# Optimization experiments

Measured on AMD Instinct MI355X. Metric: run time of the kernel, lower is better.

Reference implementation:

```python
import jax, jax.numpy as jnp
import numpy as np
import math

HIDDEN = 1024
HEADS = 16
HEAD_DIM = HIDDEN // HEADS
B, S = 2, 2048


def setup_inputs() -> dict:
    key = jax.random.key(0)
    ks = jax.random.split(key, 10)
    std = 1.0 / math.sqrt(HIDDEN)
    mk = lambda k: (jax.random.normal(k, (HIDDEN, HIDDEN), jnp.float32) * std)
    return {
        "hidden_states": jax.random.normal(ks[0], (B, S, HIDDEN), jnp.float32),
        "attention_mask": jnp.zeros((B, 1, 1, S), jnp.float32),
        "wq": mk(ks[1]), "bq": jnp.zeros((HIDDEN,), jnp.float32),
        "wk": mk(ks[2]), "bk": jnp.zeros((HIDDEN,), jnp.float32),
        "wv": mk(ks[3]), "bv": jnp.zeros((HIDDEN,), jnp.float32),
        "wo": mk(ks[4]), "bo": jnp.zeros((HIDDEN,), jnp.float32),
    }


def reference(hidden_states, attention_mask, wq, bq, wk, bk, wv, bv, wo, bo):
    b, s, _ = hidden_states.shape
    scale = math.sqrt(HEAD_DIM)
    # projections (torch Linear: x @ W.T + b); weights stored as [out, in]
    q = hidden_states @ wq.T + bq
    k = hidden_states @ wk.T + bk
    v = hidden_states @ wv.T + bv
    # [B, H, S, D]
    q = q.reshape(b, s, HEADS, HEAD_DIM).transpose(0, 2, 1, 3)
    k = k.reshape(b, s, HEADS, HEAD_DIM).transpose(0, 2, 1, 3)
    v = v.reshape(b, s, HEADS, HEAD_DIM).transpose(0, 2, 1, 3)
    scores = jnp.einsum("bhqd,bhkd->bhqk", q, k) / scale
    scores = scores + attention_mask  # broadcast [B,1,1,S]
    weights = jax.nn.softmax(scores, axis=-1)  # dropout = identity (eval)
    out = jnp.einsum("bhqk,bhkd->bhqd", weights, v)
    out = out.transpose(0, 2, 1, 3).reshape(b, s, HIDDEN)
    out = out @ wo.T + bo
    return out
```

## Files before the change

### kernel.cpp

```cpp
#include <hip/hip_runtime.h>
#include <hip/hip_bf16.h>

typedef __bf16 bf16_t;
typedef __bf16 bf16x8 __attribute__((ext_vector_type(8)));
typedef float f32x4 __attribute__((ext_vector_type(4)));

#define SEQ    2048
#define NH     16
#define HD     64
#define HIDDEN 1024
#define PSTR   72

__device__ __forceinline__ bf16_t to_bf16(float f) { return (bf16_t)f; }

__device__ __forceinline__ void async16(const bf16_t* g, bf16_t* l) {
    __builtin_amdgcn_global_load_lds((const __attribute__((address_space(1))) void*)g,
                                     (__attribute__((address_space(3))) void*)l, 16, 0, 0);
}

__global__ __launch_bounds__(256) void cvt_kernel(
    const float* __restrict__ s0, bf16_t* __restrict__ d0, int c0,
    const float* __restrict__ s1, bf16_t* __restrict__ d1, int c1,
    const float* __restrict__ s2, bf16_t* __restrict__ d2, int c2,
    const float* __restrict__ s3, bf16_t* __restrict__ d3, int c3)
{
    int blk = blockIdx.x;
    const float* s; bf16_t* d;
    if (blk < c0)              { s = s0; d = d0; }
    else if ((blk -= c0) < c1) { s = s1; d = d1; }
    else if ((blk -= c1) < c2) { s = s2; d = d2; }
    else                       { blk -= c2; s = s3; d = d3; }
    const size_t base = (size_t)blk * 2048 + threadIdx.x * 8;
    const float4 a = *(const float4*)&s[base];
    const float4 b = *(const float4*)&s[base + 4];
    bf16x8 o;
    o[0] = (bf16_t)a.x; o[1] = (bf16_t)a.y; o[2] = (bf16_t)a.z; o[3] = (bf16_t)a.w;
    o[4] = (bf16_t)b.x; o[5] = (bf16_t)b.y; o[6] = (bf16_t)b.z; o[7] = (bf16_t)b.w;
    *(bf16x8*)&d[base] = o;
}

__device__ __forceinline__ void gemm_tile(const bf16_t* __restrict__ A,
                                          const bf16_t* __restrict__ W,
                                          int m0, int n0, f32x4 acc[4][4])
{
    __shared__ __align__(16) bf16_t As[128 * 32];
    __shared__ __align__(16) bf16_t Bs[128 * 32];
    const int t = threadIdx.x, lane = t & 63, w = t >> 6;
    const int w0 = w & 1, w1 = w >> 1, l15 = lane & 15, q4 = lane >> 4;

#pragma unroll
    for (int i = 0; i < 4; i++)
#pragma unroll
        for (int j = 0; j < 4; j++) acc[i][j] = f32x4{0.f, 0.f, 0.f, 0.f};

    for (int kt = 0; kt < HIDDEN; kt += 32) {
#pragma unroll
        for (int j = 0; j < 2; j++) {
            const int s = j * 256 + t;
            const int row = s >> 2, p = s & 3, c = p ^ (row & 3);
            const int lbase = (j * 256 + w * 64) * 8;
            async16(&A[(size_t)(m0 + row) * HIDDEN + kt + c * 8], &As[lbase]);
            async16(&W[(size_t)(n0 + row) * HIDDEN + kt + c * 8], &Bs[lbase]);
        }
        __syncthreads();
        bf16x8 af[4];
#pragma unroll
        for (int ti = 0; ti < 4; ti++) {
            const int r = w0 * 64 + ti * 16 + l15;
            af[ti] = *(const bf16x8*)&As[r * 32 + (q4 ^ (r & 3)) * 8];
        }
#pragma unroll
        for (int tj = 0; tj < 4; tj++) {
            const int rb = w1 * 64 + tj * 16 + l15;
            const bf16x8 bfr = *(const bf16x8*)&Bs[rb * 32 + (q4 ^ (rb & 3)) * 8];
#pragma unroll
            for (int ti = 0; ti < 4; ti++)
                acc[ti][tj] = __builtin_amdgcn_mfma_f32_16x16x32_bf16(af[ti], bfr, acc[ti][tj], 0, 0, 0);
        }
        __syncthreads();
    }
}

__global__ __launch_bounds__(256, 3) void qkv_kernel(
    const bf16_t* __restrict__ X,
    const bf16_t* __restrict__ wq, const bf16_t* __restrict__ wk, const bf16_t* __restrict__ wv,
    const float* __restrict__ bq, const float* __restrict__ bk, const float* __restrict__ bv,
    bf16_t* __restrict__ qws, bf16_t* __restrict__ kws, bf16_t* __restrict__ vws)
{
    const int z = blockIdx.z;
    const bf16_t* Wsel = (z == 0) ? wq : (z == 1) ? wk : wv;
    const float*  bsel = (z == 0) ? bq : (z == 1) ? bk : bv;
    bf16_t* dst        = (z == 0) ? qws : (z == 1) ? kws : vws;
    const int m0 = blockIdx.y * 128, n0 = blockIdx.x * 128;

    f32x4 acc[4][4];
    gemm_tile(X, Wsel, m0, n0, acc);

    const int t = threadIdx.x, lane = t & 63, wv_ = t >> 6;
    const int w0 = wv_ & 1, w1 = wv_ >> 1, l15 = lane & 15, q4 = lane >> 4;
#pragma unroll
    for (int tj = 0; tj < 4; tj++) {
        const int n = n0 + w1 * 64 + tj * 16 + l15;
        const float bb = bsel[n];
        const int hh = n >> 6, d = n & 63;
#pragma unroll
        for (int ti = 0; ti < 4; ti++)
#pragma unroll
            for (int r = 0; r < 4; r++) {
                const int m = m0 + w0 * 64 + ti * 16 + q4 * 4 + r;
                const int b = m >> 11, s = m & (SEQ - 1);
                const float val = acc[ti][tj][r] + bb;
                if (z < 2)
                    dst[(((size_t)b * NH + hh) * SEQ + s) * HD + d] = to_bf16(val);
                else
                    dst[(((size_t)b * NH + hh) * HD + d) * SEQ + s] = to_bf16(val);
            }
    }
}

__global__ __launch_bounds__(256, 4) void attn_kernel(
    const bf16_t* __restrict__ Qw, const bf16_t* __restrict__ Kw,
    const bf16_t* __restrict__ Vtw, const float* __restrict__ Mask,
    bf16_t* __restrict__ Ow)
{
    __shared__ __align__(16) bf16_t Ks[64 * 64];
    __shared__ __align__(16) bf16_t Vs[64 * 64];
    __shared__ __align__(16) bf16_t Ps[4 * 16 * PSTR];

    const int t = threadIdx.x, lane = t & 63, w = t >> 6;
    const int l15 = lane & 15, q4 = lane >> 4;
    const int bh = blockIdx.y, b = bh >> 4, h = bh & 15;
    const int q0 = blockIdx.x * 64;
    const bf16_t* Qh = Qw  + (size_t)bh * SEQ * HD;
    const bf16_t* Kh = Kw  + (size_t)bh * SEQ * HD;
    const bf16_t* Vh = Vtw + (size_t)bh * HD * SEQ;
    const float* Mrow = Mask + (size_t)b * SEQ;

    bf16x8 qf[2];
#pragma unroll
    for (int ks = 0; ks < 2; ks++)
        qf[ks] = *(const bf16x8*)&Qh[(size_t)(q0 + w * 16 + l15) * HD + ks * 32 + q4 * 8];

    f32x4 oacc[4];
#pragma unroll
    for (int nb = 0; nb < 4; nb++) oacc[nb] = f32x4{0.f, 0.f, 0.f, 0.f};
    float psum[4] = {0.f, 0.f, 0.f, 0.f};

    for (int kt = 0; kt < SEQ; kt += 64) {
#pragma unroll
        for (int j = 0; j < 2; j++) {
            const int s = j * 256 + t;
            const int row = s >> 3, p = s & 7, c = p ^ (row & 7);
            const int lbase = (j * 256 + w * 64) * 8;
            async16(&Kh[(size_t)(kt + row) * HD + c * 8], &Ks[lbase]);
            async16(&Vh[(size_t)row * SEQ + kt + c * 8], &Vs[lbase]);
        }
        __syncthreads();

        f32x4 sa[4];
#pragma unroll
        for (int cb = 0; cb < 4; cb++) sa[cb] = f32x4{0.f, 0.f, 0.f, 0.f};
#pragma unroll
        for (int cb = 0; cb < 4; cb++)
#pragma unroll
            for (int ks = 0; ks < 2; ks++) {
                const int r = cb * 16 + l15;
                const bf16x8 kf = *(const bf16x8*)&Ks[r * 64 + (((ks * 4 + q4) ^ (r & 7))) * 8];
                sa[cb] = __builtin_amdgcn_mfma_f32_16x16x32_bf16(qf[ks], kf, sa[cb], 0, 0, 0);
            }

#pragma unroll
        for (int cb = 0; cb < 4; cb++) {
            const float mk = Mrow[kt + cb * 16 + l15];
#pragma unroll
            for (int r = 0; r < 4; r++) {
                const float p = __expf(sa[cb][r] * 0.125f + mk);
                psum[r] += p;
                Ps[(w * 16 + q4 * 4 + r) * PSTR + cb * 16 + l15] = to_bf16(p);
            }
        }

#pragma unroll
        for (int ks = 0; ks < 2; ks++) {
            const bf16x8 pf = *(const bf16x8*)&Ps[(w * 16 + l15) * PSTR + ks * 32 + q4 * 8];
#pragma unroll
            for (int nb = 0; nb < 4; nb++) {
                const int r = nb * 16 + l15;
                const bf16x8 vf = *(const bf16x8*)&Vs[r * 64 + (((ks * 4 + q4) ^ (r & 7))) * 8];
                oacc[nb] = __builtin_amdgcn_mfma_f32_16x16x32_bf16(pf, vf, oacc[nb], 0, 0, 0);
            }
        }
        __syncthreads();
    }

#pragma unroll
    for (int r = 0; r < 4; r++) {
#pragma unroll
        for (int off = 1; off < 16; off <<= 1) psum[r] += __shfl_xor(psum[r], off);
    }
#pragma unroll
    for (int r = 0; r < 4; r++) {
        const float inv = 1.f / psum[r];
        const int s = q0 + w * 16 + q4 * 4 + r;
#pragma unroll
        for (int nb = 0; nb < 4; nb++) {
            const int d = nb * 16 + l15;
            Ow[((size_t)b * SEQ + s) * HIDDEN + h * HD + d] = to_bf16(oacc[nb][r] * inv);
        }
    }
}

__global__ __launch_bounds__(256, 3) void oproj_kernel(
    const bf16_t* __restrict__ A, const bf16_t* __restrict__ Wo,
    const float* __restrict__ bo, float* __restrict__ Out)
{
    const int m0 = blockIdx.y * 128, n0 = blockIdx.x * 128;
    f32x4 acc[4][4];
    gemm_tile(A, Wo, m0, n0, acc);
    const int t = threadIdx.x, lane = t & 63, wv_ = t >> 6;
    const int w0 = wv_ & 1, w1 = wv_ >> 1, l15 = lane & 15, q4 = lane >> 4;
#pragma unroll
    for (int tj = 0; tj < 4; tj++) {
        const int n = n0 + w1 * 64 + tj * 16 + l15;
        const float bb = bo[n];
#pragma unroll
        for (int ti = 0; ti < 4; ti++)
#pragma unroll
            for (int r = 0; r < 4; r++) {
                const int m = m0 + w0 * 64 + ti * 16 + q4 * 4 + r;
                Out[(size_t)m * HIDDEN + n] = acc[ti][tj][r] + bb;
            }
    }
}

extern "C" void kernel_launch(void* const* d_in, const int* in_sizes, int n_in,
                              void* d_out, int out_size, void* d_ws, size_t ws_size,
                              hipStream_t stream) {
    const float* X   = (const float*)d_in[0];
    const float* msk = (const float*)d_in[1];
    const float* wq  = (const float*)d_in[2];
    const float* bq  = (const float*)d_in[3];
    const float* wk  = (const float*)d_in[4];
    const float* bk  = (const float*)d_in[5];
    const float* wv  = (const float*)d_in[6];
    const float* bv  = (const float*)d_in[7];
    const float* wo  = (const float*)d_in[8];
    const float* bo  = (const float*)d_in[9];
    float* out = (float*)d_out;

    const size_t NELT = (size_t)2 * SEQ * HIDDEN;
    const size_t WELT = (size_t)HIDDEN * HIDDEN;
    bf16_t* xbf = (bf16_t*)d_ws;
    bf16_t* qws = xbf + NELT;
    bf16_t* kws = qws + NELT;
    bf16_t* vws = kws + NELT;
    bf16_t* aws = xbf;
    bf16_t* wqb = (bf16_t*)d_out;
    bf16_t* wkb = wqb + WELT;
    bf16_t* wvb = wkb + WELT;
    bf16_t* wob = qws;

    cvt_kernel<<<dim3(2048 + 3 * 512), dim3(256), 0, stream>>>(
        X, xbf, 2048, wq, wqb, 512, wk, wkb, 512, wv, wvb, 512);
    qkv_kernel<<<dim3(8, 32, 3), dim3(256), 0, stream>>>(
        xbf, wqb, wkb, wvb, bq, bk, bv, qws, kws, vws);
    attn_kernel<<<dim3(32, 32), dim3(256), 0, stream>>>(qws, kws, vws, msk, aws);
    cvt_kernel<<<dim3(512), dim3(256), 0, stream>>>(
        wo, wob, 512, wo, wob, 0, wo, wob, 0, wo, wob, 0);
    oproj_kernel<<<dim3(8, 32), dim3(256), 0, stream>>>(aws, wob, bo, out);
}
```

Measured before the change: 222.1 us.

## Retile QKV/oproj GEMMs and attention, store Q/K row-major, use exp2

Result: slower. 229.5 us (+3.3%).

```diff
diff --git a/kernel.cpp b/kernel.cpp
--- a/kernel.cpp
+++ b/kernel.cpp
@@ -10,6 +10,7 @@
 #define HD     64
 #define HIDDEN 1024
 #define PSTR   72
+#define LOG2E  1.44269504f
 
 __device__ __forceinline__ bf16_t to_bf16(float f) { return (bf16_t)f; }
 
@@ -39,65 +40,59 @@
     *(bf16x8*)&d[base] = o;
 }
 
-__device__ __forceinline__ void gemm_tile(const bf16_t* __restrict__ A,
-                                          const bf16_t* __restrict__ W,
-                                          int m0, int n0, f32x4 acc[4][4])
-{
-    __shared__ __align__(16) bf16_t As[128 * 32];
-    __shared__ __align__(16) bf16_t Bs[128 * 32];
-    const int t = threadIdx.x, lane = t & 63, w = t >> 6;
-    const int w0 = w & 1, w1 = w >> 1, l15 = lane & 15, q4 = lane >> 4;
-
-#pragma unroll
-    for (int i = 0; i < 4; i++)
-#pragma unroll
-        for (int j = 0; j < 4; j++) acc[i][j] = f32x4{0.f, 0.f, 0.f, 0.f};
-
-    for (int kt = 0; kt < HIDDEN; kt += 32) {
-#pragma unroll
-        for (int j = 0; j < 2; j++) {
-            const int s = j * 256 + t;
-            const int row = s >> 2, p = s & 3, c = p ^ (row & 3);
-            const int lbase = (j * 256 + w * 64) * 8;
-            async16(&A[(size_t)(m0 + row) * HIDDEN + kt + c * 8], &As[lbase]);
-            async16(&W[(size_t)(n0 + row) * HIDDEN + kt + c * 8], &Bs[lbase]);
-        }
-        __syncthreads();
-        bf16x8 af[4];
-#pragma unroll
-        for (int ti = 0; ti < 4; ti++) {
-            const int r = w0 * 64 + ti * 16 + l15;
-            af[ti] = *(const bf16x8*)&As[r * 32 + (q4 ^ (r & 3)) * 8];
-        }
-#pragma unroll
-        for (int tj = 0; tj < 4; tj++) {
-            const int rb = w1 * 64 + tj * 16 + l15;
-            const bf16x8 bfr = *(const bf16x8*)&Bs[rb * 32 + (q4 ^ (rb & 3)) * 8];
-#pragma unroll
-            for (int ti = 0; ti < 4; ti++)
-                acc[ti][tj] = __builtin_amdgcn_mfma_f32_16x16x32_bf16(af[ti], bfr, acc[ti][tj], 0, 0, 0);
-        }
-        __syncthreads();
-    }
-}
-
 __global__ __launch_bounds__(256, 3) void qkv_kernel(
     const bf16_t* __restrict__ X,
     const bf16_t* __restrict__ wq, const bf16_t* __restrict__ wk, const bf16_t* __restrict__ wv,
     const float* __restrict__ bq, const float* __restrict__ bk, const float* __restrict__ bv,
     bf16_t* __restrict__ qws, bf16_t* __restrict__ kws, bf16_t* __restrict__ vws)
 {
+    __shared__ __align__(16) bf16_t As[128 * 64];
+    __shared__ __align__(16) bf16_t Bs[128 * 64];
     const int z = blockIdx.z;
     const bf16_t* Wsel = (z == 0) ? wq : (z == 1) ? wk : wv;
     const float*  bsel = (z == 0) ? bq : (z == 1) ? bk : bv;
     bf16_t* dst        = (z == 0) ? qws : (z == 1) ? kws : vws;
     const int m0 = blockIdx.y * 128, n0 = blockIdx.x * 128;
 
+    const int t = threadIdx.x, lane = t & 63, w = t >> 6;
+    const int w0 = w & 1, w1 = w >> 1, l15 = lane & 15, q4 = lane >> 4;
+
     f32x4 acc[4][4];
-    gemm_tile(X, Wsel, m0, n0, acc);
-
-    const int t = threadIdx.x, lane = t & 63, wv_ = t >> 6;
-    const int w0 = wv_ & 1, w1 = wv_ >> 1, l15 = lane & 15, q4 = lane >> 4;
+#pragma unroll
+    for (int i = 0; i < 4; i++)
+#pragma unroll
+        for (int j = 0; j < 4; j++) acc[i][j] = f32x4{0.f, 0.f, 0.f, 0.f};
+
+    for (int kt = 0; kt < HIDDEN; kt += 64) {
+#pragma unroll
+        for (int j = 0; j < 4; j++) {
+            const int s = j * 256 + t;
+            const int row = s >> 3, c = (s & 7) ^ (row & 7);
+            const int lbase = (j * 256 + w * 64) * 8;
+            async16(&X[(size_t)(m0 + row) * HIDDEN + kt + c * 8], &As[lbase]);
+            async16(&Wsel[(size_t)(n0 + row) * HIDDEN + kt + c * 8], &Bs[lbase]);
+        }
+        __syncthreads();
+#pragma unroll
+        for (int ks = 0; ks < 2; ks++) {
+            bf16x8 af[4];
+#pragma unroll
+            for (int ti = 0; ti < 4; ti++) {
+                const int ra = w0 * 64 + ti * 16 + l15;
+                af[ti] = *(const bf16x8*)&As[ra * 64 + (((ks * 4 + q4) ^ (ra & 7))) * 8];
+            }
+#pragma unroll
+            for (int tj = 0; tj < 4; tj++) {
+                const int rb = w1 * 64 + tj * 16 + l15;
+                const bf16x8 bfr = *(const bf16x8*)&Bs[rb * 64 + (((ks * 4 + q4) ^ (rb & 7))) * 8];
+#pragma unroll
+                for (int ti = 0; ti < 4; ti++)
+                    acc[ti][tj] = __builtin_amdgcn_mfma_f32_16x16x32_bf16(af[ti], bfr, acc[ti][tj], 0, 0, 0);
+            }
+        }
+        __syncthreads();
+    }
+
 #pragma unroll
     for (int tj = 0; tj < 4; tj++) {
         const int n = n0 + w1 * 64 + tj * 16 + l15;
@@ -108,126 +103,187 @@
 #pragma unroll
             for (int r = 0; r < 4; r++) {
                 const int m = m0 + w0 * 64 + ti * 16 + q4 * 4 + r;
-                const int b = m >> 11, s = m & (SEQ - 1);
                 const float val = acc[ti][tj][r] + bb;
-                if (z < 2)
-                    dst[(((size_t)b * NH + hh) * SEQ + s) * HD + d] = to_bf16(val);
-                else
+                if (z < 2) {
+                    dst[(size_t)m * HIDDEN + n] = to_bf16(val);
+                } else {
+                    const int b = m >> 11, s = m & (SEQ - 1);
                     dst[(((size_t)b * NH + hh) * HD + d) * SEQ + s] = to_bf16(val);
-            }
-    }
-}
-
-__global__ __launch_bounds__(256, 4) void attn_kernel(
+                }
+            }
+    }
+}
+
+__global__ __launch_bounds__(256, 2) void attn_kernel(
     const bf16_t* __restrict__ Qw, const bf16_t* __restrict__ Kw,
     const bf16_t* __restrict__ Vtw, const float* __restrict__ Mask,
     bf16_t* __restrict__ Ow)
 {
     __shared__ __align__(16) bf16_t Ks[64 * 64];
     __shared__ __align__(16) bf16_t Vs[64 * 64];
-    __shared__ __align__(16) bf16_t Ps[4 * 16 * PSTR];
+    __shared__ __align__(16) bf16_t Ps[4 * 32 * PSTR];
 
     const int t = threadIdx.x, lane = t & 63, w = t >> 6;
     const int l15 = lane & 15, q4 = lane >> 4;
-    const int bh = blockIdx.y, b = bh >> 4, h = bh & 15;
-    const int q0 = blockIdx.x * 64;
-    const bf16_t* Qh = Qw  + (size_t)bh * SEQ * HD;
-    const bf16_t* Kh = Kw  + (size_t)bh * SEQ * HD;
+    const int lid = blockIdx.x + 16 * blockIdx.y;
+    const int c8 = lid & 7, j = lid >> 3;
+    const int bh = (c8 << 2) | (j >> 4);
+    const int q0 = (j & 15) << 7;
+    const int b = bh >> 4, h = bh & 15;
+
+    const bf16_t* Qh = Qw + (size_t)b * SEQ * HIDDEN + h * HD;
+    const bf16_t* Kh = Kw + (size_t)b * SEQ * HIDDEN + h * HD;
     const bf16_t* Vh = Vtw + (size_t)bh * HD * SEQ;
     const float* Mrow = Mask + (size_t)b * SEQ;
 
-    bf16x8 qf[2];
-#pragma unroll
-    for (int ks = 0; ks < 2; ks++)
-        qf[ks] = *(const bf16x8*)&Qh[(size_t)(q0 + w * 16 + l15) * HD + ks * 32 + q4 * 8];
-
-    f32x4 oacc[4];
-#pragma unroll
-    for (int nb = 0; nb < 4; nb++) oacc[nb] = f32x4{0.f, 0.f, 0.f, 0.f};
-    float psum[4] = {0.f, 0.f, 0.f, 0.f};
+    bf16x8 qf[2][2];
+#pragma unroll
+    for (int rb = 0; rb < 2; rb++)
+#pragma unroll
+        for (int ks = 0; ks < 2; ks++)
+            qf[rb][ks] = *(const bf16x8*)&Qh[(size_t)(q0 + w * 32 + rb * 16 + l15) * HIDDEN + ks * 32 + q4 * 8];
+
+    f32x4 oacc[2][4];
+#pragma unroll
+    for (int rb = 0; rb < 2; rb++)
+#pragma unroll
+        for (int nb = 0; nb < 4; nb++) oacc[rb][nb] = f32x4{0.f, 0.f, 0.f, 0.f};
+    float psum[2][4] = {{0.f, 0.f, 0.f, 0.f}, {0.f, 0.f, 0.f, 0.f}};
 
     for (int kt = 0; kt < SEQ; kt += 64) {
 #pragma unroll
-        for (int j = 0; j < 2; j++) {
-            const int s = j * 256 + t;
-            const int row = s >> 3, p = s & 7, c = p ^ (row & 7);
-            const int lbase = (j * 256 + w * 64) * 8;
-            async16(&Kh[(size_t)(kt + row) * HD + c * 8], &Ks[lbase]);
+        for (int jj = 0; jj < 2; jj++) {
+            const int s = jj * 256 + t;
+            const int row = s >> 3, c = (s & 7) ^ (row & 7);
+            const int lbase = (jj * 256 + w * 64) * 8;
+            async16(&Kh[(size_t)(kt + row) * HIDDEN + c * 8], &Ks[lbase]);
             async16(&Vh[(size_t)row * SEQ + kt + c * 8], &Vs[lbase]);
         }
         __syncthreads();
 
-        f32x4 sa[4];
-#pragma unroll
-        for (int cb = 0; cb < 4; cb++) sa[cb] = f32x4{0.f, 0.f, 0.f, 0.f};
+        f32x4 sa[2][4];
+#pragma unroll
+        for (int rb = 0; rb < 2; rb++)
+#pragma unroll
+            for (int cb = 0; cb < 4; cb++) sa[rb][cb] = f32x4{0.f, 0.f, 0.f, 0.f};
 #pragma unroll
         for (int cb = 0; cb < 4; cb++)
 #pragma unroll
             for (int ks = 0; ks < 2; ks++) {
                 const int r = cb * 16 + l15;
                 const bf16x8 kf = *(const bf16x8*)&Ks[r * 64 + (((ks * 4 + q4) ^ (r & 7))) * 8];
-                sa[cb] = __builtin_amdgcn_mfma_f32_16x16x32_bf16(qf[ks], kf, sa[cb], 0, 0, 0);
+                sa[0][cb] = __builtin_amdgcn_mfma_f32_16x16x32_bf16(qf[0][ks], kf, sa[0][cb], 0, 0, 0);
+                sa[1][cb] = __builtin_amdgcn_mfma_f32_16x16x32_bf16(qf[1][ks], kf, sa[1][cb], 0, 0, 0);
             }
 
 #pragma unroll
         for (int cb = 0; cb < 4; cb++) {
-            const float mk = Mrow[kt + cb * 16 + l15];
-#pragma unroll
-            for (int r = 0; r < 4; r++) {
-                const float p = __expf(sa[cb][r] * 0.125f + mk);
-                psum[r] += p;
-                Ps[(w * 16 + q4 * 4 + r) * PSTR + cb * 16 + l15] = to_bf16(p);
-            }
+            const float mk2 = Mrow[kt + cb * 16 + l15] * LOG2E;
+#pragma unroll
+            for (int rb = 0; rb < 2; rb++)
+#pragma unroll
+                for (int r = 0; r < 4; r++) {
+                    const float p = exp2f(fmaf(sa[rb][cb][r], 0.125f * LOG2E, mk2));
+                    psum[rb][r] += p;
+                    Ps[(w * 32 + rb * 16 + q4 * 4 + r) * PSTR + cb * 16 + l15] = to_bf16(p);
+                }
         }
 
 #pragma unroll
         for (int ks = 0; ks < 2; ks++) {
-            const bf16x8 pf = *(const bf16x8*)&Ps[(w * 16 + l15) * PSTR + ks * 32 + q4 * 8];
+            const bf16x8 pf0 = *(const bf16x8*)&Ps[(w * 32 +      l15) * PSTR + ks * 32 + q4 * 8];
+            const bf16x8 pf1 = *(const bf16x8*)&Ps[(w * 32 + 16 + l15) * PSTR + ks * 32 + q4 * 8];
 #pragma unroll
             for (int nb = 0; nb < 4; nb++) {
-                const int r = nb * 16 + l15;
-                const bf16x8 vf = *(const bf16x8*)&Vs[r * 64 + (((ks * 4 + q4) ^ (r & 7))) * 8];
-                oacc[nb] = __builtin_amdgcn_mfma_f32_16x16x32_bf16(pf, vf, oacc[nb], 0, 0, 0);
-            }
-        }
-        __syncthreads();
-    }
-
-#pragma unroll
-    for (int r = 0; r < 4; r++) {
-#pragma unroll
-        for (int off = 1; off < 16; off <<= 1) psum[r] += __shfl_xor(psum[r], off);
-    }
-#pragma unroll
-    for (int r = 0; r < 4; r++) {
-        const float inv = 1.f / psum[r];
-        const int s = q0 + w * 16 + q4 * 4 + r;
-#pragma unroll
-        for (int nb = 0; nb < 4; nb++) {
-            const int d = nb * 16 + l15;
-            Ow[((size_t)b * SEQ + s) * HIDDEN + h * HD + d] = to_bf16(oacc[nb][r] * inv);
-        }
-    }
-}
-
-__global__ __launch_bounds__(256, 3) void oproj_kernel(
+                const int rv = nb * 16 + l15;
+                const bf16x8 vf = *(const bf16x8*)&Vs[rv * 64 + (((ks * 4 + q4) ^ (rv & 7))) * 8];
+                oacc[0][nb] = __builtin_amdgcn_mfma_f32_16x16x32_bf16(pf0, vf, oacc[0][nb], 0, 0, 0);
+                oacc[1][nb] = __builtin_amdgcn_mfma_f32_16x16x32_bf16(pf1, vf, oacc[1][nb], 0, 0, 0);
+            }
+        }
+        __syncthreads();
+    }
+
+#pragma unroll
+    for (int rb = 0; rb < 2; rb++)
+#pragma unroll
+        for (int r = 0; r < 4; r++) {
+#pragma unroll
+            for (int off = 1; off < 16; off <<= 1) psum[rb][r] += __shfl_xor(psum[rb][r], off);
+        }
+#pragma unroll
+    for (int rb = 0; rb < 2; rb++)
+#pragma unroll
+        for (int r = 0; r < 4; r++) {
+            const float inv = 1.f / psum[rb][r];
+            const int s = q0 + w * 32 + rb * 16 + q4 * 4 + r;
+#pragma unroll
+            for (int nb = 0; nb < 4; nb++) {
+                const int d = nb * 16 + l15;
+                Ow[((size_t)b * SEQ + s) * HIDDEN + h * HD + d] = to_bf16(oacc[rb][nb][r] * inv);
+            }
+        }
+}
+
+__global__ __launch_bounds__(256, 2) void oproj_kernel(
     const bf16_t* __restrict__ A, const bf16_t* __restrict__ Wo,
     const float* __restrict__ bo, float* __restrict__ Out)
 {
-    const int m0 = blockIdx.y * 128, n0 = blockIdx.x * 128;
-    f32x4 acc[4][4];
-    gemm_tile(A, Wo, m0, n0, acc);
-    const int t = threadIdx.x, lane = t & 63, wv_ = t >> 6;
-    const int w0 = wv_ & 1, w1 = wv_ >> 1, l15 = lane & 15, q4 = lane >> 4;
-#pragma unroll
-    for (int tj = 0; tj < 4; tj++) {
-        const int n = n0 + w1 * 64 + tj * 16 + l15;
+    __shared__ __align__(16) bf16_t As[64 * 64];
+    __shared__ __align__(16) bf16_t Bs[128 * 64];
+    const int m0 = blockIdx.y * 64, n0 = blockIdx.x * 128;
+    const int t = threadIdx.x, lane = t & 63, w = t >> 6;
+    const int l15 = lane & 15, q4 = lane >> 4;
+
+    f32x4 acc[4][2];
+#pragma unroll
+    for (int i = 0; i < 4; i++)
+#pragma unroll
+        for (int j = 0; j < 2; j++) acc[i][j] = f32x4{0.f, 0.f, 0.f, 0.f};
+
+    for (int kt = 0; kt < HIDDEN; kt += 64) {
+#pragma unroll
+        for (int j = 0; j < 2; j++) {
+            const int s = j * 256 + t;
+            const int row = s >> 3, c = (s & 7) ^ (row & 7);
+            async16(&A[(size_t)(m0 + row) * HIDDEN + kt + c * 8], &As[(j * 256 + w * 64) * 8]);
+        }
+#pragma unroll
+        for (int j = 0; j < 4; j++) {
+            const int s = j * 256 + t;
+            const int row = s >> 3, c = (s & 7) ^ (row & 7);
+            async16(&Wo[(size_t)(n0 + row) * HIDDEN + kt + c * 8], &Bs[(j * 256 + w * 64) * 8]);
+        }
+        __syncthreads();
+#pragma unroll
+        for (int ks = 0; ks < 2; ks++) {
+            bf16x8 af[4];
+#pragma unroll
+            for (int ti = 0; ti < 4; ti++) {
+                const int ra = ti * 16 + l15;
+                af[ti] = *(const bf16x8*)&As[ra * 64 + (((ks * 4 + q4) ^ (ra & 7))) * 8];
+            }
+#pragma unroll
+            for (int tj = 0; tj < 2; tj++) {
+                const int rb = w * 32 + tj * 16 + l15;
+                const bf16x8 bfr = *(const bf16x8*)&Bs[rb * 64 + (((ks * 4 + q4) ^ (rb & 7))) * 8];
+#pragma unroll
+                for (int ti = 0; ti < 4; ti++)
+                    acc[ti][tj] = __builtin_amdgcn_mfma_f32_16x16x32_bf16(af[ti], bfr, acc[ti][tj], 0, 0, 0);
+            }
+        }
+        __syncthreads();
+    }
+
+#pragma unroll
+    for (int tj = 0; tj < 2; tj++) {
+        const int n = n0 + w * 32 + tj * 16 + l15;
         const float bb = bo[n];
 #pragma unroll
         for (int ti = 0; ti < 4; ti++)
 #pragma unroll
             for (int r = 0; r < 4; r++) {
-                const int m = m0 + w0 * 64 + ti * 16 + q4 * 4 + r;
+                const int m = m0 + ti * 16 + q4 * 4 + r;
                 Out[(size_t)m * HIDDEN + n] = acc[ti][tj][r] + bb;
             }
     }
@@ -264,8 +320,8 @@
         X, xbf, 2048, wq, wqb, 512, wk, wkb, 512, wv, wvb, 512);
     qkv_kernel<<<dim3(8, 32, 3), dim3(256), 0, stream>>>(
         xbf, wqb, wkb, wvb, bq, bk, bv, qws, kws, vws);
-    attn_kernel<<<dim3(32, 32), dim3(256), 0, stream>>>(qws, kws, vws, msk, aws);
+    attn_kernel<<<dim3(16, 32), dim3(256), 0, stream>>>(qws, kws, vws, msk, aws);
     cvt_kernel<<<dim3(512), dim3(256), 0, stream>>>(
         wo, wob, 512, wo, wob, 0, wo, wob, 0, wo, wob, 0);
-    oproj_kernel<<<dim3(8, 32), dim3(256), 0, stream>>>(aws, wob, bo, out);
-}
+    oproj_kernel<<<dim3(8, 64), dim3(256), 0, stream>>>(aws, wob, bo, out);
+}
```
